# Performance work log

Measured on AMD Instinct MI355X. Metric: run time of the kernel, lower is better.

## Reference

```python
import jax, jax.numpy as jnp
import numpy as np

B = 128          # number of trees (batched identical perfect-binary structure)
LEAVES = 1024    # leaves per tree -> N = 2*LEAVES - 1 = 2047 nodes, heap order
D_IN = 512       # input_size
NL = 64          # num_labels


def setup_inputs() -> dict:
    key = jax.random.key(0)
    k1, k2, k3, k4 = jax.random.split(key, 4)
    N = 2 * LEAVES - 1
    hidden = jax.random.normal(k1, (B, N, D_IN), dtype=jnp.float32)
    W = jax.random.normal(k2, (D_IN, NL), dtype=jnp.float32) / np.sqrt(D_IN)
    b = jax.random.normal(k3, (NL,), dtype=jnp.float32) * 0.02
    trans = jax.random.normal(k4, (NL, NL), dtype=jnp.float32) / np.sqrt(NL)
    return {"hidden": hidden, "W": W, "b": b, "trans": trans}


def reference(hidden, W, b, trans):
    # hidden: [B, N, D] with N = 2^depth - 1 nodes in heap (level) order:
    # node i's children are 2i+1, 2i+2; level d occupies [2^d-1, 2^{d+1}-1).
    Bn, N, D = hidden.shape
    L = trans.shape[0]
    depth = int(np.log2(N + 1))  # number of levels

    # emission scores for every node at once (single_h_pred, no dense layer)
    emis = jnp.einsum('bnd,dl->bnl', hidden, W) + b  # [B, N, L]

    # leaves level
    n = 2 ** (depth - 1)
    inside = emis[:, n - 1: n - 1 + n]  # [B, n, L]

    # inside algorithm, bottom-up:
    # inside[p, a] = emis[p, a]
    #             + logsumexp_l(inside_left[l]  + trans[a, l])
    #             + logsumexp_r(inside_right[r] + trans[a, r])
    for d in range(depth - 2, -1, -1):
        n = 2 ** d
        left = inside[:, 0::2]   # [B, n, L]
        right = inside[:, 1::2]  # [B, n, L]
        lt = jax.nn.logsumexp(left[:, :, None, :] + trans[None, None, :, :], axis=-1)
        rt = jax.nn.logsumexp(right[:, :, None, :] + trans[None, None, :, :], axis=-1)
        inside = emis[:, n - 1: n - 1 + n] + lt + rt  # [B, n, L]

    return inside[:, 0]  # root inside scores, [B, L]
```

## Files before the change

kernel.cpp:

```cpp
#include <hip/hip_runtime.h>
#include <math.h>

#define B_      128
#define NNODES  2047
#define NL_     64
#define DIN     512

typedef __attribute__((ext_vector_type(8))) short short8;
typedef __attribute__((ext_vector_type(4))) float v4f;

static __device__ inline unsigned short f2bf(float x) {
    unsigned u = __float_as_uint(x);
    u = (u + 0x7FFFu + ((u >> 16) & 1u)) >> 16;
    return (unsigned short)u;
}

__global__ __launch_bounds__(256) void kexp_trans(const float* __restrict__ trans,
                                                  float* __restrict__ E) {
    int i = blockIdx.x * 256 + threadIdx.x;
    if (i < NL_ * NL_) E[i] = __expf(trans[i]);
}

__global__ __launch_bounds__(256) void kprep(const float* __restrict__ W,
                                             unsigned short* __restrict__ Wt) {
    int i = blockIdx.x * 256 + threadIdx.x;
    int k = i >> 6, n = i & 63;
    Wt[n * DIN + k] = f2bf(W[i]);
}

__global__ __launch_bounds__(256) void kgemm(const float* __restrict__ H,
                                             const unsigned short* __restrict__ Wt,
                                             const float* __restrict__ bias,
                                             float* __restrict__ emis) {
    __shared__ unsigned short Al[64 * 72];
    __shared__ unsigned short Wl[64 * 72];
    int t = threadIdx.x;
    int rowBase = blockIdx.x * 64;
    int lane = t & 63;
    int w    = t >> 6;
    int ln   = lane & 15;
    int quad = lane >> 4;

    v4f acc[4];
    #pragma unroll
    for (int i = 0; i < 4; ++i) acc[i] = (v4f){0.f, 0.f, 0.f, 0.f};

    int r   = t >> 2;
    int sub = t & 3;
    const float* hrow = H + (long)(rowBase + r) * DIN + sub * 16;
    const unsigned short* wrow = Wt + r * DIN + sub * 8;

    for (int kc = 0; kc < DIN; kc += 64) {
        __syncthreads();
        #pragma unroll
        for (int i = 0; i < 4; ++i) {
            float4 v = *(const float4*)(hrow + kc + i * 4);
            unsigned long long pk =
                (unsigned long long)f2bf(v.x)
              | ((unsigned long long)f2bf(v.y) << 16)
              | ((unsigned long long)f2bf(v.z) << 32)
              | ((unsigned long long)f2bf(v.w) << 48);
            *(unsigned long long*)&Al[r * 72 + sub * 16 + i * 4] = pk;
        }
        #pragma unroll
        for (int i = 0; i < 2; ++i) {
            uint4 wv = *(const uint4*)(wrow + kc + i * 32);
            *(uint4*)&Wl[r * 72 + sub * 8 + i * 32] = wv;
        }
        __syncthreads();
        const unsigned short* Ab = &Al[(w * 16 + ln) * 72];
        const unsigned short* Wb = &Wl[ln * 72];
        #pragma unroll
        for (int ks = 0; ks < 2; ++ks) {
            short8 af = *(const short8*)(Ab + ks * 32 + quad * 8);
            #pragma unroll
            for (int nt = 0; nt < 4; ++nt) {
                short8 bf = *(const short8*)(Wb + nt * 16 * 72 + ks * 32 + quad * 8);
                acc[nt] = __builtin_amdgcn_mfma_f32_16x16x32_bf16(af, bf, acc[nt], 0, 0, 0);
            }
        }
    }
    #pragma unroll
    for (int nt = 0; nt < 4; ++nt) {
        float bv = bias[nt * 16 + ln];
        #pragma unroll
        for (int rg = 0; rg < 4; ++rg) {
            int row = rowBase + w * 16 + quad * 4 + rg;
            emis[(long)row * NL_ + nt * 16 + ln] = acc[nt][rg] + bv;
        }
    }
}

__global__ __launch_bounds__(64, 2) void klevel(float* __restrict__ inside,
                                                const float* __restrict__ E,
                                                int d) {
    int lane   = threadIdx.x;
    int n      = 1 << d;
    int groups = (B_ << d) >> 6;
    int J      = 2048 / groups;
    int jw     = 64 / J;
    int tg     = blockIdx.x / J;
    int j0     = (blockIdx.x % J) * jw;

    int task = tg * 64 + lane;
    int b    = task >> d;
    int i    = task & (n - 1);
    int g    = n - 1 + i;
    int rowL = (b * NNODES + 2 * g + 1) << 6;
    int rowG = (b * NNODES + g) << 6;

    float el[64], er[64];
    const float4* pC = (const float4*)(inside + rowL);
    #pragma unroll
    for (int q = 0; q < 16; ++q) {
        float4 v = pC[q];
        el[4*q] = v.x; el[4*q+1] = v.y; el[4*q+2] = v.z; el[4*q+3] = v.w;
    }
    #pragma unroll
    for (int q = 0; q < 16; ++q) {
        float4 v = pC[16 + q];
        er[4*q] = v.x; er[4*q+1] = v.y; er[4*q+2] = v.z; er[4*q+3] = v.w;
    }
    float ml = el[0], mr = er[0];
    #pragma unroll
    for (int k = 1; k < 64; ++k) { ml = fmaxf(ml, el[k]); mr = fmaxf(mr, er[k]); }
    #pragma unroll
    for (int k = 0; k < 64; ++k) {
        el[k] = __expf(el[k] - ml);
        er[k] = __expf(er[k] - mr);
    }
    float mbase = ml + mr;

    for (int j4 = 0; j4 < jw; j4 += 4) {
        float res[4];
        #pragma unroll
        for (int jj = 0; jj < 4; ++jj) {
            const float4* Er = (const float4*)(E + ((j0 + j4 + jj) << 6));
            float accl = 0.f, accr = 0.f;
            #pragma unroll
            for (int q = 0; q < 16; ++q) {
                float4 e = Er[q];
                accl = fmaf(el[4*q+0], e.x, accl); accl = fmaf(el[4*q+1], e.y, accl);
                accl = fmaf(el[4*q+2], e.z, accl); accl = fmaf(el[4*q+3], e.w, accl);
                accr = fmaf(er[4*q+0], e.x, accr); accr = fmaf(er[4*q+1], e.y, accr);
                accr = fmaf(er[4*q+2], e.z, accr); accr = fmaf(er[4*q+3], e.w, accr);
            }
            res[jj] = mbase + __logf(accl) + __logf(accr);
        }
        float4* pg = (float4*)(inside + rowG + j0 + j4);
        float4 ev = *pg;
        ev.x += res[0]; ev.y += res[1]; ev.z += res[2]; ev.w += res[3];
        *pg = ev;
    }
}

__global__ __launch_bounds__(256) void ktail(float* __restrict__ inside,
                                             const float* __restrict__ E,
                                             float* __restrict__ out) {
    int b    = blockIdx.x;
    int lane = threadIdx.x & 63;
    int wid  = threadIdx.x >> 6;

    float Ereg[64];
    const float4* E4 = (const float4*)(E + lane * NL_);
    #pragma unroll
    for (int q = 0; q < 16; ++q) {
        float4 v = E4[q];
        Ereg[4*q] = v.x; Ereg[4*q+1] = v.y; Ereg[4*q+2] = v.z; Ereg[4*q+3] = v.w;
    }
    int base = b * NNODES;

    for (int d = 5; d >= 0; --d) {
        int n = 1 << d;
        for (int i = wid; i < n; i += 4) {
            int g    = n - 1 + i;
            int rowC = (base + 2 * g + 1) << 6;
            float lf = inside[rowC + lane];
            float rf = inside[rowC + 64 + lane];
            float ml = lf, mr = rf;
            #pragma unroll
            for (int s = 32; s >= 1; s >>= 1) {
                ml = fmaxf(ml, __shfl_xor(ml, s));
                mr = fmaxf(mr, __shfl_xor(mr, s));
            }
            float el = __expf(lf - ml);
            float er = __expf(rf - mr);
            float accl = 0.f, accr = 0.f;
            #pragma unroll
            for (int k = 0; k < 64; ++k) {
                float ek = __int_as_float(__builtin_amdgcn_readlane(__float_as_int(el), k));
                float rk = __int_as_float(__builtin_amdgcn_readlane(__float_as_int(er), k));
                accl = fmaf(ek, Ereg[k], accl);
                accr = fmaf(rk, Ereg[k], accr);
            }
            int rowG  = (base + g) << 6;
            float res = inside[rowG + lane] + ml + mr + __logf(accl) + __logf(accr);
            if (d == 0) out[b * NL_ + lane] = res;
            else        inside[rowG + lane] = res;
        }
        __syncthreads();
    }
}

extern "C" void kernel_launch(void* const* d_in, const int* in_sizes, int n_in,
                              void* d_out, int out_size, void* d_ws, size_t ws_size,
                              hipStream_t stream) {
    const float* hidden = (const float*)d_in[0];
    const float* W      = (const float*)d_in[1];
    const float* bias   = (const float*)d_in[2];
    const float* trans  = (const float*)d_in[3];
    float* out = (float*)d_out;
    float* E   = (float*)d_ws;
    unsigned short* Wt = (unsigned short*)(E + NL_ * NL_);
    float* inside = E + NL_ * NL_ + (DIN * NL_ / 2);

    kexp_trans<<<16, 256, 0, stream>>>(trans, E);
    kprep<<<(DIN * NL_) / 256, 256, 0, stream>>>(W, Wt);
    kgemm<<<(B_ * NNODES) / 64, 256, 0, stream>>>(hidden, Wt, bias, inside);
    for (int d = 9; d >= 6; --d)
        klevel<<<2048, 64, 0, stream>>>(inside, E, d);
    ktail<<<B_, 256, 0, stream>>>(inside, E, out);
}
```

Baseline: 825.4 us.

## Load GEMM operands directly into registers with double buffering, drop LDS staging

The emission GEMM no longer stages hidden and W tiles through shared memory with barriers. Each wave now loads its A fragments (fp32, converted to bf16 in registers) and B fragments straight from global memory, using two register buffers so the next chunk's loads are in flight while the current MFMAs run. Each block now covers 128 rows, with 32 rows per wave. The two small prep kernels are also merged into one launch. The per-lane global loads are less coalesced (32-byte segments strided by row) and W is reread by every wave, which trades LDS traffic and syncs for extra L2 pressure.

```diff
diff --git a/kernel.cpp b/kernel.cpp
--- a/kernel.cpp
+++ b/kernel.cpp
@@ -15,78 +15,110 @@
     return (unsigned short)u;
 }
 
-__global__ __launch_bounds__(256) void kexp_trans(const float* __restrict__ trans,
-                                                  float* __restrict__ E) {
+__global__ __launch_bounds__(256) void kprep(const float* __restrict__ W,
+                                             const float* __restrict__ trans,
+                                             unsigned short* __restrict__ Wt,
+                                             float* __restrict__ E) {
     int i = blockIdx.x * 256 + threadIdx.x;
     if (i < NL_ * NL_) E[i] = __expf(trans[i]);
-}
-
-__global__ __launch_bounds__(256) void kprep(const float* __restrict__ W,
-                                             unsigned short* __restrict__ Wt) {
-    int i = blockIdx.x * 256 + threadIdx.x;
     int k = i >> 6, n = i & 63;
     Wt[n * DIN + k] = f2bf(W[i]);
+}
+
+struct Abuf { float4 x0, x1, y0, y1; };
+struct Bbuf { uint4 b0, b1, b2, b3; };
+
+static __device__ inline void loadA(const float* __restrict__ a0,
+                                    const float* __restrict__ a1,
+                                    int off, Abuf& A) {
+    A.x0 = *(const float4*)(a0 + off);
+    A.x1 = *(const float4*)(a0 + off + 4);
+    A.y0 = *(const float4*)(a1 + off);
+    A.y1 = *(const float4*)(a1 + off + 4);
+}
+
+static __device__ inline void loadB(const unsigned short* __restrict__ bp,
+                                    int off, Bbuf& Bb) {
+    Bb.b0 = *(const uint4*)(bp + off);
+    Bb.b1 = *(const uint4*)(bp + off + 16 * DIN);
+    Bb.b2 = *(const uint4*)(bp + off + 32 * DIN);
+    Bb.b3 = *(const uint4*)(bp + off + 48 * DIN);
+}
+
+static __device__ inline short8 cvt8(float4 u, float4 v) {
+    short8 r;
+    unsigned short* p = (unsigned short*)&r;
+    p[0] = f2bf(u.x); p[1] = f2bf(u.y); p[2] = f2bf(u.z); p[3] = f2bf(u.w);
+    p[4] = f2bf(v.x); p[5] = f2bf(v.y); p[6] = f2bf(v.z); p[7] = f2bf(v.w);
+    return r;
+}
+
+static __device__ inline void mac(const Abuf& A, const Bbuf& Bb, v4f acc[2][4]) {
+    short8 af0 = cvt8(A.x0, A.x1);
+    short8 af1 = cvt8(A.y0, A.y1);
+    short8 bf;
+    bf = *(const short8*)&Bb.b0;
+    acc[0][0] = __builtin_amdgcn_mfma_f32_16x16x32_bf16(af0, bf, acc[0][0], 0, 0, 0);
+    acc[1][0] = __builtin_amdgcn_mfma_f32_16x16x32_bf16(af1, bf, acc[1][0], 0, 0, 0);
+    bf = *(const short8*)&Bb.b1;
+    acc[0][1] = __builtin_amdgcn_mfma_f32_16x16x32_bf16(af0, bf, acc[0][1], 0, 0, 0);
+    acc[1][1] = __builtin_amdgcn_mfma_f32_16x16x32_bf16(af1, bf, acc[1][1], 0, 0, 0);
+    bf = *(const short8*)&Bb.b2;
+    acc[0][2] = __builtin_amdgcn_mfma_f32_16x16x32_bf16(af0, bf, acc[0][2], 0, 0, 0);
+    acc[1][2] = __builtin_amdgcn_mfma_f32_16x16x32_bf16(af1, bf, acc[1][2], 0, 0, 0);
+    bf = *(const short8*)&Bb.b3;
+    acc[0][3] = __builtin_amdgcn_mfma_f32_16x16x32_bf16(af0, bf, acc[0][3], 0, 0, 0);
+    acc[1][3] = __builtin_amdgcn_mfma_f32_16x16x32_bf16(af1, bf, acc[1][3], 0, 0, 0);
 }
 
 __global__ __launch_bounds__(256) void kgemm(const float* __restrict__ H,
                                              const unsigned short* __restrict__ Wt,
                                              const float* __restrict__ bias,
                                              float* __restrict__ emis) {
-    __shared__ unsigned short Al[64 * 72];
-    __shared__ unsigned short Wl[64 * 72];
-    int t = threadIdx.x;
-    int rowBase = blockIdx.x * 64;
+    int t    = threadIdx.x;
     int lane = t & 63;
     int w    = t >> 6;
     int ln   = lane & 15;
     int quad = lane >> 4;
-
-    v4f acc[4];
-    #pragma unroll
-    for (int i = 0; i < 4; ++i) acc[i] = (v4f){0.f, 0.f, 0.f, 0.f};
-
-    int r   = t >> 2;
-    int sub = t & 3;
-    const float* hrow = H + (long)(rowBase + r) * DIN + sub * 16;
-    const unsigned short* wrow = Wt + r * DIN + sub * 8;
-
+    long rowBase = (long)blockIdx.x * 128 + w * 32;
+
+    const float* a0 = H + (rowBase + ln) * DIN + quad * 8;
+    const float* a1 = a0 + 16 * DIN;
+    const unsigned short* bp = Wt + ln * DIN + quad * 8;
+
+    v4f acc[2][4];
+    #pragma unroll
+    for (int mt = 0; mt < 2; ++mt)
+        #pragma unroll
+        for (int nt = 0; nt < 4; ++nt)
+            acc[mt][nt] = (v4f){0.f, 0.f, 0.f, 0.f};
+
+    Abuf A0, A1; Bbuf Bb0, Bb1;
+    loadA(a0, a1, 0, A0);
+    loadB(bp, 0, Bb0);
+
+    #pragma unroll
     for (int kc = 0; kc < DIN; kc += 64) {
-        __syncthreads();
-        #pragma unroll
-        for (int i = 0; i < 4; ++i) {
-            float4 v = *(const float4*)(hrow + kc + i * 4);
-            unsigned long long pk =
-                (unsigned long long)f2bf(v.x)
-              | ((unsigned long long)f2bf(v.y) << 16)
-              | ((unsigned long long)f2bf(v.z) << 32)
-              | ((unsigned long long)f2bf(v.w) << 48);
-            *(unsigned long long*)&Al[r * 72 + sub * 16 + i * 4] = pk;
-        }
-        #pragma unroll
-        for (int i = 0; i < 2; ++i) {
-            uint4 wv = *(const uint4*)(wrow + kc + i * 32);
-            *(uint4*)&Wl[r * 72 + sub * 8 + i * 32] = wv;
-        }
-        __syncthreads();
-        const unsigned short* Ab = &Al[(w * 16 + ln) * 72];
-        const unsigned short* Wb = &Wl[ln * 72];
-        #pragma unroll
-        for (int ks = 0; ks < 2; ++ks) {
-            short8 af = *(const short8*)(Ab + ks * 32 + quad * 8);
-            #pragma unroll
-            for (int nt = 0; nt < 4; ++nt) {
-                short8 bf = *(const short8*)(Wb + nt * 16 * 72 + ks * 32 + quad * 8);
-                acc[nt] = __builtin_amdgcn_mfma_f32_16x16x32_bf16(af, bf, acc[nt], 0, 0, 0);
-            }
-        }
-    }
+        loadA(a0, a1, kc + 32, A1);
+        loadB(bp, kc + 32, Bb1);
+        mac(A0, Bb0, acc);
+        if (kc + 64 < DIN) {
+            loadA(a0, a1, kc + 64, A0);
+            loadB(bp, kc + 64, Bb0);
+        }
+        mac(A1, Bb1, acc);
+    }
+
     #pragma unroll
     for (int nt = 0; nt < 4; ++nt) {
         float bv = bias[nt * 16 + ln];
         #pragma unroll
-        for (int rg = 0; rg < 4; ++rg) {
-            int row = rowBase + w * 16 + quad * 4 + rg;
-            emis[(long)row * NL_ + nt * 16 + ln] = acc[nt][rg] + bv;
+        for (int mt = 0; mt < 2; ++mt) {
+            #pragma unroll
+            for (int rg = 0; rg < 4; ++rg) {
+                long row = rowBase + mt * 16 + quad * 4 + rg;
+                emis[row * NL_ + nt * 16 + ln] = acc[mt][nt][rg] + bv;
+            }
         }
     }
 }
@@ -214,9 +246,8 @@
     unsigned short* Wt = (unsigned short*)(E + NL_ * NL_);
     float* inside = E + NL_ * NL_ + (DIN * NL_ / 2);
 
-    kexp_trans<<<16, 256, 0, stream>>>(trans, E);
-    kprep<<<(DIN * NL_) / 256, 256, 0, stream>>>(W, Wt);
-    kgemm<<<(B_ * NNODES) / 64, 256, 0, stream>>>(hidden, Wt, bias, inside);
+    kprep<<<(DIN * NL_) / 256, 256, 0, stream>>>(W, trans, Wt, E);
+    kgemm<<<(B_ * NNODES) / 128, 256, 0, stream>>>(hidden, Wt, bias, inside);
     for (int d = 9; d >= 6; --d)
         klevel<<<2048, 64, 0, stream>>>(inside, E, d);
     ktail<<<B_, 256, 0, stream>>>(inside, E, out);
```

After: 843.6 us. +2.2%, slower.

## Stage child rows in LDS and split level work across waves

Applied to the files above, without the earlier changes.

Replaces the per-lane tree-level kernel with a 256-thread block kernel. It stages 64 parents' child rows into swizzled shared memory with coalesced loads, computes the max and exp cooperatively, and splits the output labels across waves and blocks using a templated width per level. It also merges the trans-exp and W-prep kernels into one launch. The aim is to replace the strided per-lane global reads and the 128-float register arrays with shared-memory reuse and better occupancy, at the cost of 32KB of LDS per block and redundant staging when a group is split across several blocks.

```diff
diff --git a/kernel.cpp b/kernel.cpp
--- a/kernel.cpp
+++ b/kernel.cpp
@@ -15,15 +15,12 @@
     return (unsigned short)u;
 }
 
-__global__ __launch_bounds__(256) void kexp_trans(const float* __restrict__ trans,
-                                                  float* __restrict__ E) {
+__global__ __launch_bounds__(256) void kprep(const float* __restrict__ W,
+                                             const float* __restrict__ trans,
+                                             unsigned short* __restrict__ Wt,
+                                             float* __restrict__ E) {
     int i = blockIdx.x * 256 + threadIdx.x;
     if (i < NL_ * NL_) E[i] = __expf(trans[i]);
-}
-
-__global__ __launch_bounds__(256) void kprep(const float* __restrict__ W,
-                                             unsigned short* __restrict__ Wt) {
-    int i = blockIdx.x * 256 + threadIdx.x;
     int k = i >> 6, n = i & 63;
     Wt[n * DIN + k] = f2bf(W[i]);
 }
@@ -91,65 +88,114 @@
     }
 }
 
-__global__ __launch_bounds__(64, 2) void klevel(float* __restrict__ inside,
-                                                const float* __restrict__ E,
-                                                int d) {
-    int lane   = threadIdx.x;
-    int n      = 1 << d;
-    int groups = (B_ << d) >> 6;
-    int J      = 2048 / groups;
-    int jw     = 64 / J;
-    int tg     = blockIdx.x / J;
-    int j0     = (blockIdx.x % J) * jw;
-
-    int task = tg * 64 + lane;
-    int b    = task >> d;
-    int i    = task & (n - 1);
-    int g    = n - 1 + i;
-    int rowL = (b * NNODES + 2 * g + 1) << 6;
-    int rowG = (b * NNODES + g) << 6;
-
-    float el[64], er[64];
-    const float4* pC = (const float4*)(inside + rowL);
-    #pragma unroll
-    for (int q = 0; q < 16; ++q) {
-        float4 v = pC[q];
-        el[4*q] = v.x; el[4*q+1] = v.y; el[4*q+2] = v.z; el[4*q+3] = v.w;
-    }
-    #pragma unroll
-    for (int q = 0; q < 16; ++q) {
-        float4 v = pC[16 + q];
-        er[4*q] = v.x; er[4*q+1] = v.y; er[4*q+2] = v.z; er[4*q+3] = v.w;
-    }
-    float ml = el[0], mr = er[0];
-    #pragma unroll
-    for (int k = 1; k < 64; ++k) { ml = fmaxf(ml, el[k]); mr = fmaxf(mr, er[k]); }
-    #pragma unroll
-    for (int k = 0; k < 64; ++k) {
-        el[k] = __expf(el[k] - ml);
-        er[k] = __expf(er[k] - mr);
-    }
-    float mbase = ml + mr;
-
-    for (int j4 = 0; j4 < jw; j4 += 4) {
-        float res[4];
-        #pragma unroll
-        for (int jj = 0; jj < 4; ++jj) {
-            const float4* Er = (const float4*)(E + ((j0 + j4 + jj) << 6));
-            float accl = 0.f, accr = 0.f;
-            #pragma unroll
-            for (int q = 0; q < 16; ++q) {
+template<int JW>
+__global__ __launch_bounds__(256, 4) void klevel2(float* __restrict__ inside,
+                                                  const float* __restrict__ E,
+                                                  int d) {
+    constexpr int JS = 16 / JW;
+    __shared__ float Ls[128 * 64];
+    __shared__ float ms[128];
+    int t = threadIdx.x;
+    int n = 1 << d;
+    int gpb = n >> 6;
+    int group = blockIdx.x / JS;
+    int js    = blockIdx.x - group * JS;
+    int b  = group / gpb;
+    int i0 = (group - b * gpb) << 6;
+    int g0 = n - 1 + i0;
+    long cbase = ((long)(b * NNODES + 2 * g0 + 1)) << 6;
+
+    const float4* src = (const float4*)(inside + cbase);
+    #pragma unroll
+    for (int it = 0; it < 8; ++it) {
+        int q   = t + it * 256;
+        int row = q >> 4, slot = q & 15;
+        float4 v = src[q];
+        *(float4*)&Ls[row * 64 + ((slot ^ ((row >> 1) & 15)) << 2)] = v;
+    }
+    __syncthreads();
+
+    {
+        int row  = t >> 1, half = t & 1;
+        int pk   = (row >> 1) & 15;
+        float vals[32];
+        #pragma unroll
+        for (int q = 0; q < 8; ++q) {
+            int slot = half * 8 + q;
+            float4 v = *(const float4*)&Ls[row * 64 + ((slot ^ pk) << 2)];
+            vals[4*q] = v.x; vals[4*q+1] = v.y; vals[4*q+2] = v.z; vals[4*q+3] = v.w;
+        }
+        float m = vals[0];
+        #pragma unroll
+        for (int k = 1; k < 32; ++k) m = fmaxf(m, vals[k]);
+        m = fmaxf(m, __shfl_xor(m, 1));
+        #pragma unroll
+        for (int k = 0; k < 32; ++k) vals[k] = __expf(vals[k] - m);
+        #pragma unroll
+        for (int q = 0; q < 8; ++q) {
+            int slot = half * 8 + q;
+            *(float4*)&Ls[row * 64 + ((slot ^ pk) << 2)] =
+                (float4){vals[4*q], vals[4*q+1], vals[4*q+2], vals[4*q+3]};
+        }
+        if (half == 0) ms[row] = m;
+    }
+    __syncthreads();
+
+    int p  = t & 63;
+    int w  = t >> 6;
+    int j0 = (js * 4 + w) * JW;
+    float accl[JW], accr[JW];
+    #pragma unroll
+    for (int j = 0; j < JW; ++j) { accl[j] = 0.f; accr[j] = 0.f; }
+
+    #pragma unroll
+    for (int c = 0; c < 4; ++c) {
+        float el[16], er[16];
+        #pragma unroll
+        for (int q = 0; q < 4; ++q) {
+            int sl = ((c * 4 + q) ^ (p & 15)) << 2;
+            float4 v = *(const float4*)&Ls[(2 * p)     * 64 + sl];
+            float4 u = *(const float4*)&Ls[(2 * p + 1) * 64 + sl];
+            el[4*q]=v.x; el[4*q+1]=v.y; el[4*q+2]=v.z; el[4*q+3]=v.w;
+            er[4*q]=u.x; er[4*q+1]=u.y; er[4*q+2]=u.z; er[4*q+3]=u.w;
+        }
+        #pragma unroll
+        for (int j = 0; j < JW; ++j) {
+            const float4* Er = (const float4*)(E + ((j0 + j) << 6) + c * 16);
+            #pragma unroll
+            for (int q = 0; q < 4; ++q) {
                 float4 e = Er[q];
-                accl = fmaf(el[4*q+0], e.x, accl); accl = fmaf(el[4*q+1], e.y, accl);
-                accl = fmaf(el[4*q+2], e.z, accl); accl = fmaf(el[4*q+3], e.w, accl);
-                accr = fmaf(er[4*q+0], e.x, accr); accr = fmaf(er[4*q+1], e.y, accr);
-                accr = fmaf(er[4*q+2], e.z, accr); accr = fmaf(er[4*q+3], e.w, accr);
-            }
-            res[jj] = mbase + __logf(accl) + __logf(accr);
-        }
-        float4* pg = (float4*)(inside + rowG + j0 + j4);
-        float4 ev = *pg;
-        ev.x += res[0]; ev.y += res[1]; ev.z += res[2]; ev.w += res[3];
+                accl[j] = fmaf(el[4*q+0], e.x, accl[j]);
+                accl[j] = fmaf(el[4*q+1], e.y, accl[j]);
+                accl[j] = fmaf(el[4*q+2], e.z, accl[j]);
+                accl[j] = fmaf(el[4*q+3], e.w, accl[j]);
+                accr[j] = fmaf(er[4*q+0], e.x, accr[j]);
+                accr[j] = fmaf(er[4*q+1], e.y, accr[j]);
+                accr[j] = fmaf(er[4*q+2], e.z, accr[j]);
+                accr[j] = fmaf(er[4*q+3], e.w, accr[j]);
+            }
+        }
+    }
+
+    float mbase = ms[2 * p] + ms[2 * p + 1];
+    #pragma unroll
+    for (int j = 0; j < JW; ++j)
+        accl[j] = mbase + __logf(accl[j]) + __logf(accr[j]);
+
+    long prow = ((long)(b * NNODES + g0 + p)) << 6;
+    if constexpr (JW >= 4) {
+        #pragma unroll
+        for (int j4 = 0; j4 < JW; j4 += 4) {
+            float4* pg = (float4*)(inside + prow + j0 + j4);
+            float4 ev = *pg;
+            ev.x += accl[j4]; ev.y += accl[j4+1];
+            ev.z += accl[j4+2]; ev.w += accl[j4+3];
+            *pg = ev;
+        }
+    } else {
+        float2* pg = (float2*)(inside + prow + j0);
+        float2 ev = *pg;
+        ev.x += accl[0]; ev.y += accl[1];
         *pg = ev;
     }
 }
@@ -214,10 +260,11 @@
     unsigned short* Wt = (unsigned short*)(E + NL_ * NL_);
     float* inside = E + NL_ * NL_ + (DIN * NL_ / 2);
 
-    kexp_trans<<<16, 256, 0, stream>>>(trans, E);
-    kprep<<<(DIN * NL_) / 256, 256, 0, stream>>>(W, Wt);
+    kprep<<<(DIN * NL_) / 256, 256, 0, stream>>>(W, trans, Wt, E);
     kgemm<<<(B_ * NNODES) / 64, 256, 0, stream>>>(hidden, Wt, bias, inside);
-    for (int d = 9; d >= 6; --d)
-        klevel<<<2048, 64, 0, stream>>>(inside, E, d);
+    klevel2<16><<<((B_ << 9) >> 6) * 1, 256, 0, stream>>>(inside, E, 9);
+    klevel2< 8><<<((B_ << 8) >> 6) * 2, 256, 0, stream>>>(inside, E, 8);
+    klevel2< 4><<<((B_ << 7) >> 6) * 4, 256, 0, stream>>>(inside, E, 7);
+    klevel2< 2><<<((B_ << 6) >> 6) * 8, 256, 0, stream>>>(inside, E, 6);
     ktail<<<B_, 256, 0, stream>>>(inside, E, out);
 }
```

Result: no change. 812.2 us (-1.6%).
